# Kernel optimization log

Measured on AMD Instinct MI355X. Metric: run time of the kernel, lower is better.

## Reference

```python
import jax, jax.numpy as jnp
import numpy as np

N = 100000        # nodes
E_INTRA = 800000  # intra (covalent) edges
E_INTER = 400000  # inter (protein-ligand) edges
NODE_DIM = 35
H = 128           # hidden_dim
G = 256           # graphs in batch
N_LAYERS = 4
BN_EPS = 1e-5

seg_sum = jax.ops.segment_sum


def setup_inputs() -> dict:
    key = jax.random.key(0)
    ks = jax.random.split(key, 24)
    s = 1.0 / np.sqrt(H)
    inp = {
        "x": jax.random.normal(ks[0], (N, NODE_DIM), jnp.float32),
        "edge_index_intra": jax.random.randint(ks[1], (2, E_INTRA), 0, N, jnp.int32),
        "edge_index_inter": jax.random.randint(ks[2], (2, E_INTER), 0, N, jnp.int32),
        "pos": jax.random.normal(ks[3], (N, 3), jnp.float32),
        "edge_attr": jax.random.uniform(ks[4], (E_INTRA, 1), jnp.float32),
        "batch": jnp.sort(jax.random.randint(ks[5], (N,), 0, G, jnp.int32)),
        # lin_node
        "lin_node_W": jax.random.normal(ks[6], (NODE_DIM, H), jnp.float32) / np.sqrt(NODE_DIM),
        "lin_node_b": jnp.zeros((H,), jnp.float32),
        # 4 DVNHIL layers (stacked)
        "W_intra": jax.random.normal(ks[7], (N_LAYERS, H, H), jnp.float32) * s,
        "b_intra": jnp.zeros((N_LAYERS, H), jnp.float32),
        "W_inter": jax.random.normal(ks[8], (N_LAYERS, H, H), jnp.float32) * s,
        "b_inter": jnp.zeros((N_LAYERS, H), jnp.float32),
        # FC head: 3 hidden linears + BN affine, then output linear to 1 task
        "fc_W": jax.random.normal(ks[9], (3, H, H), jnp.float32) * s,
        "fc_b": jnp.zeros((3, H), jnp.float32),
        "bn_gamma": jnp.ones((3, H), jnp.float32),
        "bn_beta": jnp.zeros((3, H), jnp.float32),
        "out_W": jax.random.normal(ks[10], (H, 1), jnp.float32) * s,
        "out_b": jnp.zeros((1,), jnp.float32),
    }
    return inp


def reference(x, edge_index_intra, edge_index_inter, pos, edge_attr, batch,
              lin_node_W, lin_node_b, W_intra, b_intra, W_inter, b_inter,
              fc_W, fc_b, bn_gamma, bn_beta, out_W, out_b):
    src_i, dst_i = edge_index_intra[0], edge_index_intra[1]
    src_e, dst_e = edge_index_inter[0], edge_index_inter[1]

    # lin_node: Linear + SiLU
    h = jax.nn.silu(x @ lin_node_W + lin_node_b)  # [N, H]

    # degrees of destination nodes (scatter-add of ones)
    ones_i = jnp.ones((src_i.shape[0],), h.dtype)
    ones_e = jnp.ones((src_e.shape[0],), h.dtype)
    deg_intra = seg_sum(ones_i, dst_i, num_segments=N)[:, None]           # [N,1]
    deg_inter = jnp.log(seg_sum(ones_e, dst_e, num_segments=N)[:, None] + 1.0)

    # geometric weight on inter edges from pos
    d2 = jnp.sum((pos[src_e] - pos[dst_e]) ** 2, axis=-1, keepdims=True)  # [E_inter,1]
    w_inter = jnp.exp(-d2)

    v_p = jnp.zeros_like(h)
    v_l = jnp.zeros_like(h)
    for i in range(N_LAYERS):
        # intra: gather -> edge-weighted transform -> scatter-add -> degree norm
        m_i = (h[src_i] * edge_attr) @ W_intra[i] + b_intra[i]            # [E_intra,H]
        m_i = seg_sum(m_i, dst_i, num_segments=N) / (deg_intra + 1.0)
        # inter: gather -> distance-weighted transform -> scatter-add -> log-degree scale
        m_e = (h[src_e] * w_inter) @ W_inter[i] + b_inter[i]              # [E_inter,H]
        m_e = seg_sum(m_e, dst_e, num_segments=N) * deg_inter
        v_p = jax.nn.silu(m_i + v_p)
        v_l = jax.nn.silu(m_e + v_l)
        h = h + v_p + v_l

    # global_add_pool over graphs
    g = seg_sum(h, batch, num_segments=G)  # [G, H]

    # FC head (eval mode: dropout identity, BN with running mean=0/var=1)
    bn_scale = 1.0 / jnp.sqrt(1.0 + BN_EPS)
    for j in range(3):
        g = jax.nn.leaky_relu(g @ fc_W[j] + fc_b[j], negative_slope=0.01)
        g = g * bn_scale * bn_gamma[j] + bn_beta[j]
    out = g @ out_W + out_b  # [G, 1]
    return out.reshape(-1)
```

## Files before the change

kernel.cpp:

```cpp
#include <hip/hip_runtime.h>
#include <math.h>

#define NN 100000
#define EIN 800000
#define EEX 400000
#define ND 35
#define H 128
#define NG 256
#define NL 4
#define TM 16
#define TML 16
#define NTILES 6250
#define CAPI 32
#define CAPE 16
#define OVFCAP 16384
#define EPT 4

typedef unsigned short u16;
typedef unsigned char u8;
typedef short s8v __attribute__((ext_vector_type(8)));
typedef float f4v __attribute__((ext_vector_type(4)));
typedef float f2v __attribute__((ext_vector_type(2)));

__device__ __forceinline__ float silu_f(float x){ return x / (1.0f + __expf(-x)); }
__device__ __forceinline__ float bf2f(u16 v){ return __uint_as_float(((unsigned)v) << 16); }
__device__ __forceinline__ float bfw_lo(unsigned u){ return __uint_as_float(u << 16); }
__device__ __forceinline__ float bfw_hi(unsigned u){ return __uint_as_float(u & 0xffff0000u); }
__device__ __forceinline__ u16 f2bf(float f){
  unsigned u = __float_as_uint(f);
  u += 0x7FFFu + ((u >> 16) & 1u);
  return (u16)(u >> 16);
}
__device__ __forceinline__ u8 f2fp8(float f){
  int p = __builtin_amdgcn_cvt_pk_fp8_f32(f, f, 0, false);
  return (u8)(p & 0xff);
}
__device__ __forceinline__ unsigned pk_bf16(float lo, float hi){
  unsigned r;
  asm("v_cvt_pk_bf16_f32 %0, %1, %2" : "=v"(r) : "v"(lo), "v"(hi));
  return r;
}
__device__ __forceinline__ unsigned pack_ew(int s, float w){
  return ((unsigned)s << 15) | (unsigned)f2bf(w);
}

__global__ __launch_bounds__(256) void k_prep(const float* __restrict__ x,
                                              const float* __restrict__ lnW,
                                              const float* __restrict__ lnb,
                                              u16* __restrict__ h,
                                              u8* __restrict__ h8,
                                              const float* __restrict__ WI,
                                              const float* __restrict__ WE,
                                              u16* __restrict__ WfI,
                                              u16* __restrict__ WfE,
                                              const int* __restrict__ src_i,
                                              const int* __restrict__ dst_i,
                                              const float* __restrict__ ea,
                                              const int* __restrict__ src_e,
                                              const int* __restrict__ dst_e,
                                              const float* __restrict__ pos,
                                              int* __restrict__ cnt_i,
                                              int* __restrict__ cnt_e,
                                              unsigned* __restrict__ bktI,
                                              unsigned* __restrict__ bktE,
                                              int* __restrict__ ovfhdr,
                                              int4* __restrict__ ovfList){
  const int NBW = 2*NL;
  const int NBL = NN/TML;
  if (blockIdx.x < NBW){
    const int lm = blockIdx.x;
    const int l = lm >> 1;
    const float* src = (lm & 1) ? (WE + (size_t)l*H*H) : (WI + (size_t)l*H*H);
    u16* dst = ((lm & 1) ? WfE : WfI) + (size_t)l*H*H;
    for (int idx = threadIdx.x; idx < H*H; idx += 256){
      const int r = idx & 7, lane = (idx>>3)&63, kc = (idx>>9)&3, jt = idx>>11;
      const int k = kc*32 + (lane>>4)*8 + r;
      const int j = jt*16 + (lane&15);
      dst[idx] = f2bf(src[k*H + j]);
    }
    return;
  }
  if (blockIdx.x < NBW + NBL){
    __shared__ u16 xs[TM][72];
    const int n0 = (blockIdx.x - NBW) * TML;
    const int tid = threadIdx.x;
    for (int i = tid; i < TM*64; i += 256){
      const int m = i >> 6, k = i & 63;
      xs[m][k] = (k < ND) ? f2bf(x[(size_t)(n0+m)*ND + k]) : (u16)0;
    }
    __syncthreads();
    const int lane = tid & 63;
    const int wv   = tid >> 6;
    const int col  = lane & 15;
    const int quad = lane >> 4;
    const int jta = 2*wv, jtb = 2*wv + 1;
    const int ja = jta*16 + col, jb = jtb*16 + col;

    f4v accA = {0.f,0.f,0.f,0.f}, accB = {0.f,0.f,0.f,0.f};
    #pragma unroll
    for (int kc = 0; kc < 2; ++kc){
      const s8v a = *(const s8v*)&xs[col][kc*32 + quad*8];
      s8v bA, bB;
      #pragma unroll
      for (int r = 0; r < 8; ++r){
        const int k = kc*32 + quad*8 + r;
        bA[r] = (k < ND) ? (short)f2bf(lnW[k*H + ja]) : (short)0;
        bB[r] = (k < ND) ? (short)f2bf(lnW[k*H + jb]) : (short)0;
      }
      accA = __builtin_amdgcn_mfma_f32_16x16x32_bf16(a, bA, accA, 0, 0, 0);
      accB = __builtin_amdgcn_mfma_f32_16x16x32_bf16(a, bB, accB, 0, 0, 0);
    }
    const float bja = lnb[ja], bjb = lnb[jb];
    #pragma unroll
    for (int r = 0; r < 4; ++r){
      const int n = n0 + quad*4 + r;
      const float ha = silu_f(accA[r] + bja);
      const float hb = silu_f(accB[r] + bjb);
      h[(size_t)n*H + ja] = f2bf(ha);
      h[(size_t)n*H + jb] = f2bf(hb);
      h8[(size_t)n*H + ja] = f2fp8(ha);
      h8[(size_t)n*H + jb] = f2fp8(hb);
    }
    return;
  }
  const int NE_ALL_ = EIN + EEX;
  const int base = (blockIdx.x - NBW - NBL)*(256*EPT) + (int)threadIdx.x;
  int eV[EPT], sV[EPT], dV[EPT];
  #pragma unroll
  for (int k = 0; k < EPT; ++k){
    const int e = base + k*256;
    eV[k] = e;
    int s = 0, d = 0;
    if (e < EIN){ s = src_i[e]; d = dst_i[e]; }
    else if (e < NE_ALL_){ s = src_e[e-EIN]; d = dst_e[e-EIN]; }
    sV[k] = s; dV[k] = d;
  }
  float wV[EPT];
  #pragma unroll
  for (int k = 0; k < EPT; ++k){
    const int e = eV[k];
    float w = 0.f;
    if (e < EIN) w = ea[e];
    else if (e < NE_ALL_){
      const int s = sV[k], d = dV[k];
      const float dx = pos[3*s+0] - pos[3*d+0];
      const float dy = pos[3*s+1] - pos[3*d+1];
      const float dz = pos[3*s+2] - pos[3*d+2];
      w = __expf(-(dx*dx + dy*dy + dz*dz));
    }
    wV[k] = w;
  }
  #pragma unroll
  for (int k = 0; k < EPT; ++k){
    const int e = eV[k];
    if (e < EIN){
      const int slot = atomicAdd(&cnt_i[dV[k]], 1);
      if (slot < CAPI) bktI[((size_t)dV[k] << 5) + slot] = pack_ew(sV[k], wV[k]);
      else {
        const int oi = atomicAdd(ovfhdr, 1);
        if (oi < OVFCAP) ovfList[oi] = make_int4(dV[k], sV[k], __float_as_int(wV[k]), 0);
      }
    } else if (e < NE_ALL_){
      const int slot = atomicAdd(&cnt_e[dV[k]], 1);
      if (slot < CAPE) bktE[((size_t)dV[k] << 4) + slot] = pack_ew(sV[k], wV[k]);
      else {
        const int oi = atomicAdd(ovfhdr, 1);
        if (oi < OVFCAP) ovfList[oi] = make_int4(dV[k], sV[k], __float_as_int(wV[k]), 1);
      }
    }
  }
}

#define ACCONE(qx, qy, vv, A0, A1, A2, A3) {                                          \
    const f2v x01 = __builtin_amdgcn_cvt_pk_f32_fp8((int)(qx), false);                \
    const f2v x23 = __builtin_amdgcn_cvt_pk_f32_fp8((int)(qx), true);                 \
    const f2v x45 = __builtin_amdgcn_cvt_pk_f32_fp8((int)(qy), false);                \
    const f2v x67 = __builtin_amdgcn_cvt_pk_f32_fp8((int)(qy), true);                 \
    A0 += x01 * (vv); A1 += x23 * (vv); A2 += x45 * (vv); A3 += x67 * (vv); }

#define GATHER_SHARED_DECL                                                            \
  __shared__ __align__(16) char smem_[16896];                                         \
  u16 (*aggIs)[136] = (u16(*)[136])(smem_);                                           \
  u16 (*aggEs)[136] = (u16(*)[136])(smem_ + 4352);                                    \
  unsigned (*edI)[CAPI] = (unsigned(*)[CAPI])(smem_ + 8704);      \
  unsigned (*edE)[CAPE] = (unsigned(*)[CAPE])(smem_ + 10752);     \
  float (*mif)[132] = (float(*)[132])(smem_);                                         \
  float (*mef)[132] = (float(*)[132])(smem_ + 8448);

#define GATHER_DECLS                                                                  \
  const int slot = tid >> 4;                                                          \
  const int l16  = tid & 15;                                                          \
  const int j8 = l16 * 8;                                                             \
  const int n = n0 + slot;                                                            \
  const int cIv = cntI[n];                                                            \
  const int cEv = cntE[n];

#define GATHER_LDS_BODY                                                               \
  {                                                                                   \
    const int uI = cIv < CAPI ? cIv : CAPI;                                           \
    const int uE = cEv < CAPE ? cEv : CAPE;                                           \
    const int pIv = (uI + 7) & ~7;                                                    \
    const int pEv = (uE + 3) & ~3;                                                    \
    {                                                                                 \
      const size_t bI_ = ((size_t)n << 5);                                            \
      for (int t = l16; t < pIv; t += 16)                                             \
        edI[slot][t] = (t < uI) ? bktI[bI_ + t] : 0u;                                 \
      const size_t bE_ = ((size_t)n << 4);                                            \
      if (l16 < pEv)                                                                  \
        edE[slot][l16] = (l16 < uE) ? bktE[bE_ + l16] : 0u;                           \
    }                                                                                 \
    __syncthreads();                                                                  \
    f2v aI0={0.f,0.f}, aI1={0.f,0.f}, aI2={0.f,0.f}, aI3={0.f,0.f};                   \
    f2v aE0={0.f,0.f}, aE1={0.f,0.f}, aE2={0.f,0.f}, aE3={0.f,0.f};                   \
    {                                                                                 \
      const int nbI_ = pIv >> 3, nbE_ = pEv >> 2;                                     \
      const int nb = nbI_ > nbE_ ? nbI_ : nbE_;                                       \
      int tIi = 0, tEi = 0;                                                           \
      for (int b = 0; b < nb; ++b){                                                   \
        const bool doI = b < nbI_;                                                    \
        const bool doE = b < nbE_;                                                    \
        unsigned eIw[8], eEw[4]; uint2 qI[8], qE[4];                                  \
        if (doI){                                                                     \
          *(uint4*)&eIw[0] = *(const uint4*)&edI[slot][tIi+0];                        \
          *(uint4*)&eIw[4] = *(const uint4*)&edI[slot][tIi+4];                        \
          _Pragma("unroll")                                                           \
          for (int k = 0; k < 8; ++k){                                                \
            const unsigned off = ((eIw[k] >> 15) << 7) | (unsigned)j8;                \
            qI[k] = *(const uint2*)(hin8 + off);                                      \
          }                                                                           \
        }                                                                             \
        if (doE){                                                                     \
          *(uint4*)&eEw[0] = *(const uint4*)&edE[slot][tEi+0];                        \
          _Pragma("unroll")                                                           \
          for (int k = 0; k < 4; ++k){                                                \
            const unsigned off = ((eEw[k] >> 15) << 7) | (unsigned)j8;                \
            qE[k] = *(const uint2*)(hin8 + off);                                      \
          }                                                                           \
        }                                                                             \
        if (doI){                                                                     \
          _Pragma("unroll")                                                           \
          for (int k = 0; k < 8; ++k){                                                \
            const float v = __uint_as_float((eIw[k] & 0x7fffu) << 16);                \
            ACCONE(qI[k].x, qI[k].y, v, aI0, aI1, aI2, aI3)                           \
          }                                                                           \
          tIi += 8;                                                                   \
        }                                                                             \
        if (doE){                                                                     \
          _Pragma("unroll")                                                           \
          for (int k = 0; k < 4; ++k){                                                \
            const float v = __uint_as_float((eEw[k] & 0x7fffu) << 16);                \
            ACCONE(qE[k].x, qE[k].y, v, aE0, aE1, aE2, aE3)                           \
          }                                                                           \
          tEi += 4;                                                                   \
        }                                                                             \
      }                                                                               \
    }                                                                                 \
    const int nov = ovfhdr[0];                                                        \
    if (__builtin_expect(nov > 0, 0)){                                                \
      const int novc = nov < OVFCAP ? nov : OVFCAP;                                   \
      for (int o = 0; o < novc; ++o){                                                 \
        const int4 E = ovfList[o];                                                    \
        if (E.x == n){                                                                \
          const unsigned off = ((unsigned)E.y << 7) | (unsigned)j8;                   \
          const uint2 q = *(const uint2*)(hin8 + off);                                \
          const float v = __int_as_float(E.z);                                        \
          if (E.w == 0){ ACCONE(q.x, q.y, v, aI0, aI1, aI2, aI3) }                    \
          else         { ACCONE(q.x, q.y, v, aE0, aE1, aE2, aE3) }                    \
        }                                                                             \
      }                                                                               \
    }                                                                                 \
    *(uint4*)&aggIs[slot][j8] = make_uint4(pk_bf16(aI0.x, aI0.y), pk_bf16(aI1.x, aI1.y), \
                                           pk_bf16(aI2.x, aI2.y), pk_bf16(aI3.x, aI3.y)); \
    *(uint4*)&aggEs[slot][j8] = make_uint4(pk_bf16(aE0.x, aE0.y), pk_bf16(aE1.x, aE1.y), \
                                           pk_bf16(aE2.x, aE2.y), pk_bf16(aE3.x, aE3.y)); \
  }

#define MFMA_BODY                                                                     \
  f4v accIA = {0.f,0.f,0.f,0.f}, accIB = {0.f,0.f,0.f,0.f};                           \
  f4v accEA = {0.f,0.f,0.f,0.f}, accEB = {0.f,0.f,0.f,0.f};                           \
  _Pragma("unroll")                                                                   \
  for (int kc = 0; kc < 4; ++kc){                                                     \
    const int koff = kc*32 + quad*8;                                                  \
    const s8v aI = *(const s8v*)&aggIs[col][koff];                                    \
    const s8v aE = *(const s8v*)&aggEs[col][koff];                                    \
    const s8v bIA = *(const s8v*)(WfI + (((jta*4 + kc)*64 + lane) << 3));             \
    const s8v bIB = *(const s8v*)(WfI + (((jtb*4 + kc)*64 + lane) << 3));             \
    const s8v bEA = *(const s8v*)(WfE + (((jta*4 + kc)*64 + lane) << 3));             \
    const s8v bEB = *(const s8v*)(WfE + (((jtb*4 + kc)*64 + lane) << 3));             \
    accIA = __builtin_amdgcn_mfma_f32_16x16x32_bf16(aI, bIA, accIA, 0, 0, 0);         \
    accIB = __builtin_amdgcn_mfma_f32_16x16x32_bf16(aI, bIB, accIB, 0, 0, 0);         \
    accEA = __builtin_amdgcn_mfma_f32_16x16x32_bf16(aE, bEA, accEA, 0, 0, 0);         \
    accEB = __builtin_amdgcn_mfma_f32_16x16x32_bf16(aE, bEB, accEB, 0, 0, 0);         \
  }

#define ACC2LDS                                                                       \
  __syncthreads();                                                                    \
  _Pragma("unroll")                                                                   \
  for (int r = 0; r < 4; ++r){                                                        \
    mif[quad*4+r][jta*16+col] = accIA[r];                                             \
    mif[quad*4+r][jtb*16+col] = accIB[r];                                             \
    mef[quad*4+r][jta*16+col] = accEA[r];                                             \
    mef[quad*4+r][jtb*16+col] = accEB[r];                                             \
  }                                                                                   \
  __syncthreads();

#define EPI_COMMON                                                                    \
  const float cIf = (float)cIv;                                                       \
  const float cEf = (float)cEv;                                                       \
  const float rdI = 1.0f / (cIf + 1.0f);                                              \
  const float ldE = __logf(cEf + 1.0f);                                               \
  const f4v miA = *(const f4v*)&mif[slot][j8];                                        \
  const f4v miB = *(const f4v*)&mif[slot][j8+4];                                      \
  const f4v meA = *(const f4v*)&mef[slot][j8];                                        \
  const f4v meB = *(const f4v*)&mef[slot][j8+4];                                      \
  const f4v bIa_ = *(const f4v*)(bI + j8);                                            \
  const f4v bIb_ = *(const f4v*)(bI + j8 + 4);                                        \
  const f4v bEa_ = *(const f4v*)(bE + j8);                                            \
  const f4v bEb_ = *(const f4v*)(bE + j8 + 4);                                        \
  const unsigned idx8 = (unsigned)n*H + (unsigned)j8;

#define STORE_STATE8                                                                  \
  uint4 vps, vls, hs;                                                                 \
  vps.x = pk_bf16(vpn[0],vpn[1]); vps.y = pk_bf16(vpn[2],vpn[3]);                     \
  vps.z = pk_bf16(vpn[4],vpn[5]); vps.w = pk_bf16(vpn[6],vpn[7]);                     \
  vls.x = pk_bf16(vln[0],vln[1]); vls.y = pk_bf16(vln[2],vln[3]);                     \
  vls.z = pk_bf16(vln[4],vln[5]); vls.w = pk_bf16(vln[6],vln[7]);                     \
  hs.x = pk_bf16(hnew[0],hnew[1]); hs.y = pk_bf16(hnew[2],hnew[3]);                   \
  hs.z = pk_bf16(hnew[4],hnew[5]); hs.w = pk_bf16(hnew[6],hnew[7]);                   \
  *(uint4*)(vp + idx8) = vps;                                                         \
  *(uint4*)(vl + idx8) = vls;                                                         \
  *(uint4*)(hout + idx8) = hs;                                                        \
  int d0_ = __builtin_amdgcn_cvt_pk_fp8_f32(hnew[0], hnew[1], 0, false);              \
  d0_ = __builtin_amdgcn_cvt_pk_fp8_f32(hnew[2], hnew[3], d0_, true);                 \
  int d1_ = __builtin_amdgcn_cvt_pk_fp8_f32(hnew[4], hnew[5], 0, false);              \
  d1_ = __builtin_amdgcn_cvt_pk_fp8_f32(hnew[6], hnew[7], d1_, true);                 \
  uint2 h8s; h8s.x = (unsigned)d0_; h8s.y = (unsigned)d1_;                            \
  *(uint2*)(hout8 + idx8) = h8s;

__global__ __launch_bounds__(256, 4) void k_layer(
    const u16* __restrict__ hin, const u8* __restrict__ hin8,
    u16* __restrict__ hout, u8* __restrict__ hout8,
    u16* __restrict__ vp, u16* __restrict__ vl,
    const int* __restrict__ cntI, const int* __restrict__ cntE,
    const unsigned* __restrict__ bktI, const unsigned* __restrict__ bktE,
    const int* __restrict__ ovfhdr, const int4* __restrict__ ovfList,
    const u16* __restrict__ WfI, const float* __restrict__ bI,
    const u16* __restrict__ WfE, const float* __restrict__ bE)
{
  GATHER_SHARED_DECL
  const int n0 = blockIdx.x * TM;
  const int tid = threadIdx.x;
  GATHER_DECLS
  GATHER_LDS_BODY
  __syncthreads();

  const int lane = tid & 63;
  const int w    = tid >> 6;
  const int jta = 2*w, jtb = 2*w + 1;
  const int col  = lane & 15;
  const int quad = lane >> 4;
  MFMA_BODY
  ACC2LDS

  EPI_COMMON
  const uint4 vpq = *(const uint4*)(vp + idx8);
  const uint4 vlq = *(const uint4*)(vl + idx8);
  const uint4 hq  = *(const uint4*)(hin + idx8);
  const unsigned vpw[4] = {vpq.x, vpq.y, vpq.z, vpq.w};
  const unsigned vlw[4] = {vlq.x, vlq.y, vlq.z, vlq.w};
  const unsigned hwv[4] = {hq.x, hq.y, hq.z, hq.w};
  float vpn[8], vln[8], hnew[8];
  #pragma unroll
  for (int k = 0; k < 8; ++k){
    const float miv = (k < 4) ? miA[k] : miB[k-4];
    const float mev = (k < 4) ? meA[k] : meB[k-4];
    const float bIv = (k < 4) ? bIa_[k] : bIb_[k-4];
    const float bEv = (k < 4) ? bEa_[k] : bEb_[k-4];
    const float mi = (miv + cIf*bIv) * rdI;
    const float me = (mev + cEf*bEv) * ldE;
    const float vpo = (k & 1) ? bfw_hi(vpw[k>>1]) : bfw_lo(vpw[k>>1]);
    const float vlo = (k & 1) ? bfw_hi(vlw[k>>1]) : bfw_lo(vlw[k>>1]);
    const float ho  = (k & 1) ? bfw_hi(hwv[k>>1]) : bfw_lo(hwv[k>>1]);
    vpn[k] = silu_f(mi + vpo);
    vln[k] = silu_f(me + vlo);
    hnew[k] = ho + vpn[k] + vln[k];
  }
  STORE_STATE8
}

__global__ __launch_bounds__(256, 4) void k_layer0(
    const u16* __restrict__ hin, const u8* __restrict__ hin8,
    u16* __restrict__ hout, u8* __restrict__ hout8,
    u16* __restrict__ vp, u16* __restrict__ vl,
    const int* __restrict__ cntI, const int* __restrict__ cntE,
    const unsigned* __restrict__ bktI, const unsigned* __restrict__ bktE,
    const int* __restrict__ ovfhdr, const int4* __restrict__ ovfList,
    const u16* __restrict__ WfI, const float* __restrict__ bI,
    const u16* __restrict__ WfE, const float* __restrict__ bE)
{
  GATHER_SHARED_DECL
  const int n0 = blockIdx.x * TM;
  const int tid = threadIdx.x;
  GATHER_DECLS
  GATHER_LDS_BODY
  __syncthreads();

  const int lane = tid & 63;
  const int w    = tid >> 6;
  const int jta = 2*w, jtb = 2*w + 1;
  const int col  = lane & 15;
  const int quad = lane >> 4;
  MFMA_BODY
  ACC2LDS

  EPI_COMMON
  const uint4 hq = *(const uint4*)(hin + idx8);
  const unsigned hwv[4] = {hq.x, hq.y, hq.z, hq.w};
  float vpn[8], vln[8], hnew[8];
  #pragma unroll
  for (int k = 0; k < 8; ++k){
    const float miv = (k < 4) ? miA[k] : miB[k-4];
    const float mev = (k < 4) ? meA[k] : meB[k-4];
    const float bIv = (k < 4) ? bIa_[k] : bIb_[k-4];
    const float bEv = (k < 4) ? bEa_[k] : bEb_[k-4];
    const float mi = (miv + cIf*bIv) * rdI;
    const float me = (mev + cEf*bEv) * ldE;
    const float ho = (k & 1) ? bfw_hi(hwv[k>>1]) : bfw_lo(hwv[k>>1]);
    vpn[k] = silu_f(mi);
    vln[k] = silu_f(me);
    hnew[k] = ho + vpn[k] + vln[k];
  }
  STORE_STATE8
}

__global__ __launch_bounds__(256, 4) void k_layer3(
    const u16* __restrict__ hin, const u8* __restrict__ hin8,
    u16* __restrict__ vp, u16* __restrict__ vl,
    const int* __restrict__ cntI, const int* __restrict__ cntE,
    const unsigned* __restrict__ bktI, const unsigned* __restrict__ bktE,
    const int* __restrict__ ovfhdr, const int4* __restrict__ ovfList,
    const u16* __restrict__ WfI, const float* __restrict__ bI,
    const u16* __restrict__ WfE, const float* __restrict__ bE,
    const int* __restrict__ batch, float* __restrict__ gp)
{
  GATHER_SHARED_DECL
  const int n0 = blockIdx.x * TM;
  const int tid = threadIdx.x;
  GATHER_DECLS
  GATHER_LDS_BODY
  __syncthreads();

  const int lane = tid & 63;
  const int w    = tid >> 6;
  const int jta = 2*w, jtb = 2*w + 1;
  const int col  = lane & 15;
  const int quad = lane >> 4;
  MFMA_BODY
  ACC2LDS

  EPI_COMMON
  const uint4 vpq = *(const uint4*)(vp + idx8);
  const uint4 vlq = *(const uint4*)(vl + idx8);
  const uint4 hq  = *(const uint4*)(hin + idx8);
  const unsigned vpw[4] = {vpq.x, vpq.y, vpq.z, vpq.w};
  const unsigned vlw[4] = {vlq.x, vlq.y, vlq.z, vlq.w};
  const unsigned hwv[4] = {hq.x, hq.y, hq.z, hq.w};
  float hnew[8];
  #pragma unroll
  for (int k = 0; k < 8; ++k){
    const float miv = (k < 4) ? miA[k] : miB[k-4];
    const float mev = (k < 4) ? meA[k] : meB[k-4];
    const float bIv = (k < 4) ? bIa_[k] : bIb_[k-4];
    const float bEv = (k < 4) ? bEa_[k] : bEb_[k-4];
    const float mi = (miv + cIf*bIv) * rdI;
    const float me = (mev + cEf*bEv) * ldE;
    const float vpo = (k & 1) ? bfw_hi(vpw[k>>1]) : bfw_lo(vpw[k>>1]);
    const float vlo = (k & 1) ? bfw_hi(vlw[k>>1]) : bfw_lo(vlw[k>>1]);
    const float ho  = (k & 1) ? bfw_hi(hwv[k>>1]) : bfw_lo(hwv[k>>1]);
    const float vpn = silu_f(mi + vpo);
    const float vln = silu_f(me + vlo);
    hnew[k] = ho + vpn + vln;
  }

  const int b0 = batch[n0];
  const int b15 = batch[n0 + TM - 1];
  if (b0 == b15){
    #pragma unroll
    for (int k = 0; k < 8; ++k){
      hnew[k] += __shfl_xor(hnew[k], 16, 64);
      hnew[k] += __shfl_xor(hnew[k], 32, 64);
    }
    __syncthreads();
    if (quad == 0){
      f4v s0 = {hnew[0], hnew[1], hnew[2], hnew[3]};
      f4v s1 = {hnew[4], hnew[5], hnew[6], hnew[7]};
      *(f4v*)&mif[w][j8] = s0;
      *(f4v*)&mif[w][j8+4] = s1;
    }
    __syncthreads();
    if (tid < 128){
      const float s = mif[0][tid] + mif[1][tid] + mif[2][tid] + mif[3][tid];
      atomicAdd(&gp[(size_t)b0*H + tid], s);
    }
  } else {
    const int bn = batch[n];
    #pragma unroll
    for (int k = 0; k < 8; ++k)
      atomicAdd(&gp[(size_t)bn*H + j8 + k], hnew[k]);
  }
}

__global__ void k_fc(const float* __restrict__ g, const float* __restrict__ fcW,
                     const float* __restrict__ fcb, const float* __restrict__ gamma,
                     const float* __restrict__ beta, const float* __restrict__ outW,
                     const float* __restrict__ outb, float* __restrict__ out){
  __shared__ float row[H];
  __shared__ float red[H];
  const int gi = blockIdx.x;
  const int j = threadIdx.x;
  row[j] = g[(size_t)gi*H + j];
  __syncthreads();
  const float bn_scale = rsqrtf(1.0f + 1e-5f);
  for (int l = 0; l < 3; ++l){
    const float* W = fcW + (size_t)l*H*H;
    float acc = fcb[l*H + j];
    #pragma unroll 8
    for (int k = 0; k < H; ++k) acc += row[k] * W[k*H + j];
    acc = (acc > 0.f) ? acc : 0.01f*acc;
    acc = acc * bn_scale * gamma[l*H + j] + beta[l*H + j];
    __syncthreads();
    row[j] = acc;
    __syncthreads();
  }
  red[j] = row[j] * outW[j];
  __syncthreads();
  for (int o = 64; o > 0; o >>= 1){
    if (j < o) red[j] += red[j + o];
    __syncthreads();
  }
  if (j == 0) out[gi] = red[0] + outb[0];
}

extern "C" void kernel_launch(void* const* d_in, const int* in_sizes, int n_in,
                              void* d_out, int out_size, void* d_ws, size_t ws_size,
                              hipStream_t stream)
{
  const float* x    = (const float*)d_in[0];
  const int*   eii  = (const int*)  d_in[1];
  const int*   eie  = (const int*)  d_in[2];
  const float* pos  = (const float*)d_in[3];
  const float* ea   = (const float*)d_in[4];
  const int*   batch= (const int*)  d_in[5];
  const float* lnW  = (const float*)d_in[6];
  const float* lnb  = (const float*)d_in[7];
  const float* WIa  = (const float*)d_in[8];
  const float* bIa  = (const float*)d_in[9];
  const float* WEa  = (const float*)d_in[10];
  const float* bEa  = (const float*)d_in[11];
  const float* fcW  = (const float*)d_in[12];
  const float* fcb  = (const float*)d_in[13];
  const float* gam  = (const float*)d_in[14];
  const float* bet  = (const float*)d_in[15];
  const float* outW = (const float*)d_in[16];
  const float* outb = (const float*)d_in[17];
  float* out = (float*)d_out;

  const int* src_i = eii;  const int* dst_i = eii + EIN;
  const int* src_e = eie;  const int* dst_e = eie + EEX;

  const size_t NH = (size_t)NN * H;
  u16* hA = (u16*)d_ws;
  u16* hB = hA + NH;
  u16* vp = hB + NH;
  u16* vl = vp + NH;
  u8* hA8 = (u8*)(vl + NH);
  u8* hB8 = hA8 + NH;
  float* gp = (float*)(hB8 + NH);
  int* cnt_i = (int*)(gp + (size_t)NG*H);
  int* cnt_e = cnt_i + NN;
  int* ovfhdr = cnt_e + NN;
  int4* ovfList = (int4*)(ovfhdr + 4);
  unsigned* bktI = (unsigned*)(ovfList + OVFCAP);
  unsigned* bktE = bktI + (size_t)NN*CAPI;
  u16* WfI = (u16*)(bktE + (size_t)NN*CAPE);
  u16* WfE = WfI + (size_t)NL*H*H;

  const size_t need = (size_t)((char*)(WfE + (size_t)NL*H*H) - (char*)d_ws);
  if (ws_size < need) return;

  hipMemsetAsync(gp, 0, ((size_t)NG*H + 2*(size_t)NN + 4)*sizeof(int), stream);

  const int NE_ALL = EIN + EEX;
  const int NBF = (NE_ALL + 256*EPT - 1)/(256*EPT);
  k_prep<<<2*NL + NN/TML + NBF, 256, 0, stream>>>(x, lnW, lnb, hA, hA8, WIa, WEa, WfI, WfE,
                                                  src_i, dst_i, ea, src_e, dst_e, pos,
                                                  cnt_i, cnt_e, bktI, bktE, ovfhdr, ovfList);

  k_layer0<<<NTILES, 256, 0, stream>>>(hA, hA8, hB, hB8, vp, vl,
      cnt_i, cnt_e, bktI, bktE, ovfhdr, ovfList,
      WfI + 0*(size_t)H*H, bIa + 0*H, WfE + 0*(size_t)H*H, bEa + 0*H);
  k_layer<<<NTILES, 256, 0, stream>>>(hB, hB8, hA, hA8, vp, vl,
      cnt_i, cnt_e, bktI, bktE, ovfhdr, ovfList,
      WfI + 1*(size_t)H*H, bIa + 1*H, WfE + 1*(size_t)H*H, bEa + 1*H);
  k_layer<<<NTILES, 256, 0, stream>>>(hA, hA8, hB, hB8, vp, vl,
      cnt_i, cnt_e, bktI, bktE, ovfhdr, ovfList,
      WfI + 2*(size_t)H*H, bIa + 2*H, WfE + 2*(size_t)H*H, bEa + 2*H);
  k_layer3<<<NTILES, 256, 0, stream>>>(hB, hB8, vp, vl,
      cnt_i, cnt_e, bktI, bktE, ovfhdr, ovfList,
      WfI + 3*(size_t)H*H, bIa + 3*H, WfE + 3*(size_t)H*H, bEa + 3*H,
      batch, gp);

  k_fc<<<NG, H, 0, stream>>>(gp, fcW, fcb, gam, bet, outW, outb, out);
}
```

Baseline: 440.4 us.

## Read bucket edge lists directly from global and store aggregates as bf16 in LDS

The gather loop no longer stages each node's intra and inter edge buckets in shared memory behind a __syncthreads; it reads the packed edge words straight from the global bucket rows. For those reads to be safe past the valid count, the setup memset now zeroes all bucket storage as well as the counters. The per-tile message results written to LDS after the matrix step are stored as bf16 instead of fp32. Together these shrink the shared allocation from about 16.9 KB to 8.7 KB to allow more resident blocks and drop one barrier. The cost is a much larger memset each call and extra rounding of the aggregated messages before bias, normalisation and SiLU.

```diff
diff --git a/kernel.cpp b/kernel.cpp
--- a/kernel.cpp
+++ b/kernel.cpp
@@ -179,13 +179,12 @@
     A0 += x01 * (vv); A1 += x23 * (vv); A2 += x45 * (vv); A3 += x67 * (vv); }
 
 #define GATHER_SHARED_DECL                                                            \
-  __shared__ __align__(16) char smem_[16896];                                         \
+  __shared__ __align__(16) char smem_[8704];                                          \
   u16 (*aggIs)[136] = (u16(*)[136])(smem_);                                           \
   u16 (*aggEs)[136] = (u16(*)[136])(smem_ + 4352);                                    \
-  unsigned (*edI)[CAPI] = (unsigned(*)[CAPI])(smem_ + 8704);      \
-  unsigned (*edE)[CAPE] = (unsigned(*)[CAPE])(smem_ + 10752);     \
-  float (*mif)[132] = (float(*)[132])(smem_);                                         \
-  float (*mef)[132] = (float(*)[132])(smem_ + 8448);
+  u16 (*mifh)[136] = (u16(*)[136])(smem_);                                            \
+  u16 (*mefh)[136] = (u16(*)[136])(smem_ + 4352);                                     \
+  float (*pf)[132] = (float(*)[132])(smem_);
 
 #define GATHER_DECLS                                                                  \
   const int slot = tid >> 4;                                                          \
@@ -201,15 +200,8 @@
     const int uE = cEv < CAPE ? cEv : CAPE;                                           \
     const int pIv = (uI + 7) & ~7;                                                    \
     const int pEv = (uE + 3) & ~3;                                                    \
-    {                                                                                 \
-      const size_t bI_ = ((size_t)n << 5);                                            \
-      for (int t = l16; t < pIv; t += 16)                                             \
-        edI[slot][t] = (t < uI) ? bktI[bI_ + t] : 0u;                                 \
-      const size_t bE_ = ((size_t)n << 4);                                            \
-      if (l16 < pEv)                                                                  \
-        edE[slot][l16] = (l16 < uE) ? bktE[bE_ + l16] : 0u;                           \
-    }                                                                                 \
-    __syncthreads();                                                                  \
+    const unsigned* rowIp = bktI + ((size_t)n << 5);                                  \
+    const unsigned* rowEp = bktE + ((size_t)n << 4);                                  \
     f2v aI0={0.f,0.f}, aI1={0.f,0.f}, aI2={0.f,0.f}, aI3={0.f,0.f};                   \
     f2v aE0={0.f,0.f}, aE1={0.f,0.f}, aE2={0.f,0.f}, aE3={0.f,0.f};                   \
     {                                                                                 \
@@ -221,8 +213,8 @@
         const bool doE = b < nbE_;                                                    \
         unsigned eIw[8], eEw[4]; uint2 qI[8], qE[4];                                  \
         if (doI){                                                                     \
-          *(uint4*)&eIw[0] = *(const uint4*)&edI[slot][tIi+0];                        \
-          *(uint4*)&eIw[4] = *(const uint4*)&edI[slot][tIi+4];                        \
+          *(uint4*)&eIw[0] = *(const uint4*)(rowIp + tIi);                            \
+          *(uint4*)&eIw[4] = *(const uint4*)(rowIp + tIi + 4);                        \
           _Pragma("unroll")                                                           \
           for (int k = 0; k < 8; ++k){                                                \
             const unsigned off = ((eIw[k] >> 15) << 7) | (unsigned)j8;                \
@@ -230,7 +222,7 @@
           }                                                                           \
         }                                                                             \
         if (doE){                                                                     \
-          *(uint4*)&eEw[0] = *(const uint4*)&edE[slot][tEi+0];                        \
+          *(uint4*)&eEw[0] = *(const uint4*)(rowEp + tEi);                            \
           _Pragma("unroll")                                                           \
           for (int k = 0; k < 4; ++k){                                                \
             const unsigned off = ((eEw[k] >> 15) << 7) | (unsigned)j8;                \
@@ -297,10 +289,10 @@
   __syncthreads();                                                                    \
   _Pragma("unroll")                                                                   \
   for (int r = 0; r < 4; ++r){                                                        \
-    mif[quad*4+r][jta*16+col] = accIA[r];                                             \
-    mif[quad*4+r][jtb*16+col] = accIB[r];                                             \
-    mef[quad*4+r][jta*16+col] = accEA[r];                                             \
-    mef[quad*4+r][jtb*16+col] = accEB[r];                                             \
+    mifh[quad*4+r][jta*16+col] = f2bf(accIA[r]);                                      \
+    mifh[quad*4+r][jtb*16+col] = f2bf(accIB[r]);                                      \
+    mefh[quad*4+r][jta*16+col] = f2bf(accEA[r]);                                      \
+    mefh[quad*4+r][jtb*16+col] = f2bf(accEB[r]);                                      \
   }                                                                                   \
   __syncthreads();
 
@@ -309,15 +301,18 @@
   const float cEf = (float)cEv;                                                       \
   const float rdI = 1.0f / (cIf + 1.0f);                                              \
   const float ldE = __logf(cEf + 1.0f);                                               \
-  const f4v miA = *(const f4v*)&mif[slot][j8];                                        \
-  const f4v miB = *(const f4v*)&mif[slot][j8+4];                                      \
-  const f4v meA = *(const f4v*)&mef[slot][j8];                                        \
-  const f4v meB = *(const f4v*)&mef[slot][j8+4];                                      \
+  const uint4 miq = *(const uint4*)&mifh[slot][j8];                                   \
+  const uint4 meq = *(const uint4*)&mefh[slot][j8];                                   \
+  const unsigned miw[4] = {miq.x, miq.y, miq.z, miq.w};                               \
+  const unsigned mew[4] = {meq.x, meq.y, meq.z, meq.w};                               \
   const f4v bIa_ = *(const f4v*)(bI + j8);                                            \
   const f4v bIb_ = *(const f4v*)(bI + j8 + 4);                                        \
   const f4v bEa_ = *(const f4v*)(bE + j8);                                            \
   const f4v bEb_ = *(const f4v*)(bE + j8 + 4);                                        \
   const unsigned idx8 = (unsigned)n*H + (unsigned)j8;
+
+#define MI_AT(k) ((k & 1) ? bfw_hi(miw[k>>1]) : bfw_lo(miw[k>>1]))
+#define ME_AT(k) ((k & 1) ? bfw_hi(mew[k>>1]) : bfw_lo(mew[k>>1]))
 
 #define STORE_STATE8                                                                  \
   uint4 vps, vls, hs;                                                                 \
@@ -372,12 +367,10 @@
   float vpn[8], vln[8], hnew[8];
   #pragma unroll
   for (int k = 0; k < 8; ++k){
-    const float miv = (k < 4) ? miA[k] : miB[k-4];
-    const float mev = (k < 4) ? meA[k] : meB[k-4];
     const float bIv = (k < 4) ? bIa_[k] : bIb_[k-4];
     const float bEv = (k < 4) ? bEa_[k] : bEb_[k-4];
-    const float mi = (miv + cIf*bIv) * rdI;
-    const float me = (mev + cEf*bEv) * ldE;
+    const float mi = (MI_AT(k) + cIf*bIv) * rdI;
+    const float me = (ME_AT(k) + cEf*bEv) * ldE;
     const float vpo = (k & 1) ? bfw_hi(vpw[k>>1]) : bfw_lo(vpw[k>>1]);
     const float vlo = (k & 1) ? bfw_hi(vlw[k>>1]) : bfw_lo(vlw[k>>1]);
     const float ho  = (k & 1) ? bfw_hi(hwv[k>>1]) : bfw_lo(hwv[k>>1]);
@@ -419,12 +412,10 @@
   float vpn[8], vln[8], hnew[8];
   #pragma unroll
   for (int k = 0; k < 8; ++k){
-    const float miv = (k < 4) ? miA[k] : miB[k-4];
-    const float mev = (k < 4) ? meA[k] : meB[k-4];
     const float bIv = (k < 4) ? bIa_[k] : bIb_[k-4];
     const float bEv = (k < 4) ? bEa_[k] : bEb_[k-4];
-    const float mi = (miv + cIf*bIv) * rdI;
-    const float me = (mev + cEf*bEv) * ldE;
+    const float mi = (MI_AT(k) + cIf*bIv) * rdI;
+    const float me = (ME_AT(k) + cEf*bEv) * ldE;
     const float ho = (k & 1) ? bfw_hi(hwv[k>>1]) : bfw_lo(hwv[k>>1]);
     vpn[k] = silu_f(mi);
     vln[k] = silu_f(me);
@@ -468,12 +459,10 @@
   float hnew[8];
   #pragma unroll
   for (int k = 0; k < 8; ++k){
-    const float miv = (k < 4) ? miA[k] : miB[k-4];
-    const float mev = (k < 4) ? meA[k] : meB[k-4];
     const float bIv = (k < 4) ? bIa_[k] : bIb_[k-4];
     const float bEv = (k < 4) ? bEa_[k] : bEb_[k-4];
-    const float mi = (miv + cIf*bIv) * rdI;
-    const float me = (mev + cEf*bEv) * ldE;
+    const float mi = (MI_AT(k) + cIf*bIv) * rdI;
+    const float me = (ME_AT(k) + cEf*bEv) * ldE;
     const float vpo = (k & 1) ? bfw_hi(vpw[k>>1]) : bfw_lo(vpw[k>>1]);
     const float vlo = (k & 1) ? bfw_hi(vlw[k>>1]) : bfw_lo(vlw[k>>1]);
     const float ho  = (k & 1) ? bfw_hi(hwv[k>>1]) : bfw_lo(hwv[k>>1]);
@@ -494,12 +483,12 @@
     if (quad == 0){
       f4v s0 = {hnew[0], hnew[1], hnew[2], hnew[3]};
       f4v s1 = {hnew[4], hnew[5], hnew[6], hnew[7]};
-      *(f4v*)&mif[w][j8] = s0;
-      *(f4v*)&mif[w][j8+4] = s1;
+      *(f4v*)&pf[w][j8] = s0;
+      *(f4v*)&pf[w][j8+4] = s1;
     }
     __syncthreads();
     if (tid < 128){
-      const float s = mif[0][tid] + mif[1][tid] + mif[2][tid] + mif[3][tid];
+      const float s = pf[0][tid] + pf[1][tid] + pf[2][tid] + pf[3][tid];
       atomicAdd(&gp[(size_t)b0*H + tid], s);
     }
   } else {
@@ -588,7 +577,8 @@
   const size_t need = (size_t)((char*)(WfE + (size_t)NL*H*H) - (char*)d_ws);
   if (ws_size < need) return;
 
-  hipMemsetAsync(gp, 0, ((size_t)NG*H + 2*(size_t)NN + 4)*sizeof(int), stream);
+  const size_t z_bytes = (size_t)((char*)(bktE + (size_t)NN*CAPE) - (char*)gp);
+  hipMemsetAsync(gp, 0, z_bytes, stream);
 
   const int NE_ALL = EIN + EEX;
   const int NBF = (NE_ALL + 256*EPT - 1)/(256*EPT);
```

Result: slower. 449.9 us (+2.2%).
